# Kernel tuning notes

Measured on AMD Instinct MI355X. Metric: run time of the kernel, lower is better.

## Reference

```python
import jax, jax.numpy as jnp
import numpy as np

B, T, C, H = 4, 2048, 1024, 16
HD = C // H  # head dim = 64


def setup_inputs() -> dict:
    key = jax.random.key(0)
    k1, k2, k3 = jax.random.split(key, 3)
    scale_in = 1.0 / np.sqrt(C)
    return {
        "x": jax.random.normal(k1, (B, T, C), dtype=jnp.float32),
        "W_attn": jax.random.normal(k2, (C, 3 * C), dtype=jnp.float32) * scale_in,
        "b_attn": jnp.zeros((3 * C,), dtype=jnp.float32),
        "W_proj": jax.random.normal(k3, (C, C), dtype=jnp.float32) * scale_in,
        "b_proj": jnp.zeros((C,), dtype=jnp.float32),
    }


def reference(x, W_attn, b_attn, W_proj, b_proj):
    Bx, Tx, Cx = x.shape
    qkv = x @ W_attn + b_attn                      # [B,T,3C]
    q, k, v = jnp.split(qkv, 3, axis=-1)           # each [B,T,C]
    # [B,T,C] -> [B,H,T,HD]
    q = q.reshape(Bx, Tx, H, HD).transpose(0, 2, 1, 3)
    k = k.reshape(Bx, Tx, H, HD).transpose(0, 2, 1, 3)
    v = v.reshape(Bx, Tx, H, HD).transpose(0, 2, 1, 3)
    att = jnp.einsum("bhqd,bhkd->bhqk", q, k) * (1.0 / np.sqrt(HD))
    causal = jnp.tril(jnp.ones((Tx, Tx), dtype=bool))  # [T,T]
    att = jnp.where(causal[None, None, :, :], att, jnp.float32(-jnp.inf))
    att = jax.nn.softmax(att, axis=-1)
    y = jnp.einsum("bhqk,bhkd->bhqd", att, v)      # [B,H,T,HD]
    y = y.transpose(0, 2, 1, 3).reshape(Bx, Tx, Cx)
    return y @ W_proj + b_proj
```

## Files before the change

kernel.cpp:

```cpp
#include <hip/hip_runtime.h>

typedef _Float16 f16;
typedef __attribute__((ext_vector_type(8))) _Float16 h8;
typedef __attribute__((ext_vector_type(4))) _Float16 h4;
typedef __attribute__((ext_vector_type(4))) float f4;
typedef __attribute__((ext_vector_type(16))) float f16x;
typedef __attribute__((ext_vector_type(4))) unsigned u4;

#define MFMA(a, b, c) __builtin_amdgcn_mfma_f32_16x16x32_f16(a, b, c, 0, 0, 0)
#define MFMA32(a, b, c) __builtin_amdgcn_mfma_f32_32x32x16_f16(a, b, c, 0, 0, 0)

#define QSCALE 0.18033688011112042f

__device__ __forceinline__ void gload16(const void* g, void* l) {
    __builtin_amdgcn_global_load_lds((const __attribute__((address_space(1))) void*)g,
                                     (__attribute__((address_space(3))) void*)l, 16, 0, 0);
}

__device__ __forceinline__ float fexp2(float x) {
    float r;
    asm("v_exp_f32 %0, %1" : "=v"(r) : "v"(x));
    return r;
}

__device__ __forceinline__ unsigned pkh(float a, float b) {
    auto r = __builtin_amdgcn_cvt_pkrtz(a, b);
    return __builtin_bit_cast(unsigned, r);
}

__device__ __forceinline__ void plswap(unsigned& a, unsigned& b) {
    asm volatile("v_permlane32_swap_b32 %0, %1" : "+v"(a), "+v"(b));
}


__global__ __launch_bounds__(256) void cvt_f16_kernel(const float* __restrict__ in,
                                                      f16* __restrict__ out, int n8) {
    int i = blockIdx.x * blockDim.x + threadIdx.x;
    if (i >= n8) return;
    const float4* p = (const float4*)in + (size_t)i * 2;
    float4 a = p[0], b = p[1];
    h8 o;
    o[0] = (f16)a.x; o[1] = (f16)a.y; o[2] = (f16)a.z; o[3] = (f16)a.w;
    o[4] = (f16)b.x; o[5] = (f16)b.y; o[6] = (f16)b.z; o[7] = (f16)b.w;
    *((h8*)out + i) = o;
}

__global__ __launch_bounds__(256) void transpose_cvt(const float* __restrict__ in,
                                                     f16* __restrict__ out, int R, int Cc) {
    __shared__ float tile[32][33];
    int tx = threadIdx.x, ty = threadIdx.y;
    int c0 = blockIdx.x * 32, r0 = blockIdx.y * 32;
#pragma unroll
    for (int k = 0; k < 32; k += 8)
        tile[ty + k][tx] = in[(size_t)(r0 + ty + k) * Cc + c0 + tx];
    __syncthreads();
#pragma unroll
    for (int k = 0; k < 32; k += 8)
        out[(size_t)(c0 + ty + k) * R + r0 + tx] = (f16)tile[tx][ty + k];
}


__device__ __forceinline__ void gemm_core(const f16* __restrict__ A, const f16* __restrict__ Bt,
                                          int K, int m0, int n0,
                                          f16* lA, f16* lB, f4 acc[4][4]) {
    const int tid = threadIdx.x, lane = tid & 63, wave = tid >> 6;
    const int wm = (wave >> 1) * 64, wn = (wave & 1) * 64;
    for (int k0 = 0; k0 < K; k0 += 64) {
        __syncthreads();
#pragma unroll
        for (int i = 0; i < 4; i++) {
            int s = i * 256 + wave * 64 + lane;
            int row = s >> 3;
            int gc = ((s & 7) ^ (row & 7)) * 8;
            gload16(A + (size_t)(m0 + row) * K + k0 + gc, lA + (i * 256 + wave * 64) * 8);
        }
#pragma unroll
        for (int i = 0; i < 4; i++) {
            int s = i * 256 + wave * 64 + lane;
            int row = s >> 3;
            int gc = ((s & 7) ^ (row & 7)) * 8;
            gload16(Bt + (size_t)(n0 + row) * K + k0 + gc, lB + (i * 256 + wave * 64) * 8);
        }
        __syncthreads();
#pragma unroll
        for (int kk = 0; kk < 2; kk++) {
            h8 af[4], bg[4];
#pragma unroll
            for (int im = 0; im < 4; im++) {
                int row = wm + im * 16 + (lane & 15);
                int pc = (kk * 4 + (lane >> 4)) ^ (row & 7);
                af[im] = *(const h8*)(lA + row * 64 + pc * 8);
            }
#pragma unroll
            for (int in = 0; in < 4; in++) {
                int row = wn + in * 16 + (lane & 15);
                int pc = (kk * 4 + (lane >> 4)) ^ (row & 7);
                bg[in] = *(const h8*)(lB + row * 64 + pc * 8);
            }
#pragma unroll
            for (int im = 0; im < 4; im++)
#pragma unroll
                for (int in = 0; in < 4; in++)
                    acc[im][in] = MFMA(af[im], bg[in], acc[im][in]);
        }
    }
}


__global__ __launch_bounds__(256) void qkv_gemm(const f16* __restrict__ A, const f16* __restrict__ Bt,
                                                const float* __restrict__ bias,
                                                f16* __restrict__ Qo, f16* __restrict__ Ko,
                                                f16* __restrict__ Vo) {
    __shared__ f16 lA[128 * 64], lB[128 * 64];
    f4 acc[4][4];
    const f4 zz = {0.f, 0.f, 0.f, 0.f};
#pragma unroll
    for (int i = 0; i < 4; i++)
#pragma unroll
        for (int j = 0; j < 4; j++) acc[i][j] = zz;

    const int swz = (blockIdx.x & 7) * 192 + (blockIdx.x >> 3);
    const int nb = swz % 24, mb = swz / 24;
    gemm_core(A, Bt, 1024, mb * 128, nb * 128, lA, lB, acc);

    const int lane = threadIdx.x & 63, wave = threadIdx.x >> 6;
    const int wm = (wave >> 1) * 64, wn = (wave & 1) * 64;
#pragma unroll
    for (int im = 0; im < 4; im++) {
        int m4 = mb * 128 + wm + im * 16 + (lane >> 4) * 4;
        int b = m4 >> 11, t0 = m4 & 2047;
#pragma unroll
        for (int in = 0; in < 4; in++) {
            int n = nb * 128 + wn + in * 16 + (lane & 15);
            float bb = bias[n];
            int sec = n >> 10, cc = n & 1023, hh = cc >> 6, d = cc & 63;
            if (sec == 2) {
                h4 pv;
#pragma unroll
                for (int r = 0; r < 4; r++) pv[r] = (f16)(acc[im][in][r] + bb);
                *(h4*)(Vo + ((size_t)(b * 16 + hh) * 64 + d) * 2048 + t0) = pv;
            } else {
                f16* dst = sec ? Ko : Qo;
                float sc = sec ? 1.0f : QSCALE;
                size_t base = ((size_t)(b * 16 + hh) * 2048 + t0) * 64 + d;
#pragma unroll
                for (int r = 0; r < 4; r++)
                    dst[base + (size_t)r * 64] = (f16)((acc[im][in][r] + bb) * sc);
            }
        }
    }
}


__global__ __launch_bounds__(256) void proj_gemm(const f16* __restrict__ A, const f16* __restrict__ Bt,
                                                 const float* __restrict__ bias,
                                                 float* __restrict__ out) {
    __shared__ f16 lA[128 * 64], lB[128 * 64];
    f4 acc[4][4];
    const f4 zz = {0.f, 0.f, 0.f, 0.f};
#pragma unroll
    for (int i = 0; i < 4; i++)
#pragma unroll
        for (int j = 0; j < 4; j++) acc[i][j] = zz;

    const int swz = (blockIdx.x & 7) * 64 + (blockIdx.x >> 3);
    const int nb = swz & 7, mb = swz >> 3;
    gemm_core(A, Bt, 1024, mb * 128, nb * 128, lA, lB, acc);

    const int lane = threadIdx.x & 63, wave = threadIdx.x >> 6;
    const int wm = (wave >> 1) * 64, wn = (wave & 1) * 64;
#pragma unroll
    for (int im = 0; im < 4; im++) {
        int m4 = mb * 128 + wm + im * 16 + (lane >> 4) * 4;
#pragma unroll
        for (int in = 0; in < 4; in++) {
            int n = nb * 128 + wn + in * 16 + (lane & 15);
            float bb = bias[n];
#pragma unroll
            for (int r = 0; r < 4; r++)
                out[(size_t)(m4 + r) * 1024 + n] = acc[im][in][r] + bb;
        }
    }
}


#define ASM_VMCNT(N) asm volatile("s_waitcnt vmcnt(" #N ")" ::: "memory")

__device__ __forceinline__ void attn_tile(int k0, bool last, bool stage_next,
                                          int lane, int hi, int ln,
                                          const f16* __restrict__ Kb, const f16* __restrict__ Vb,
                                          const f16* lKcur, f16* lKnxt,
                                          const h8 (&qf)[4], h8 (&vf)[2][2], h8 (&vfn)[2][2],
                                          float& mrun, float& lpart, f16x& y0, f16x& y1) {
    if (stage_next) {
#pragma unroll
        for (int i = 0; i < 4; i++) {
            int s = i * 64 + lane;
            int row = s >> 3;
            int gc = ((s & 7) ^ (row & 7)) * 8;
            gload16(Kb + (size_t)(k0 + 32 + row) * 64 + gc, lKnxt + i * 512);
        }
#pragma unroll
        for (int ks = 0; ks < 2; ks++)
#pragma unroll
            for (int j = 0; j < 2; j++)
                vfn[ks][j] = *(const h8*)(Vb + (size_t)(j * 32 + ln) * 2048 + (k0 + 32) +
                                          ks * 16 + hi * 8);
        ASM_VMCNT(8);
    } else {
        ASM_VMCNT(0);
    }
    __builtin_amdgcn_sched_barrier(0);

    f16x s0;
#pragma unroll
    for (int r = 0; r < 16; r++) s0[r] = 0.f;
    __builtin_amdgcn_s_setprio(1);
#pragma unroll
    for (int dd = 0; dd < 4; dd++) {
        const int c = (dd * 2 + hi) ^ (ln & 7);
        h8 ka = *(const h8*)(lKcur + ln * 64 + c * 8);
        s0 = MFMA32(ka, qf[dd], s0);
    }
    __builtin_amdgcn_s_setprio(0);

    if (last) {
#pragma unroll
        for (int r = 0; r < 16; r++) {
            int kl = (r & 3) + 8 * (r >> 2) + 4 * hi;
            if (kl > ln) s0[r] = -3e38f;
        }
    }

    float vmax = s0[0];
#pragma unroll
    for (int r = 1; r < 16; r++) vmax = fmaxf(vmax, s0[r]);
    vmax = fmaxf(vmax, __shfl_xor(vmax, 32));
    if (!__all(vmax <= mrun + 8.0f)) {
        float mnew = fmaxf(mrun, vmax);
        float sc = fexp2(mrun - mnew);
        lpart *= sc;
        mrun = mnew;
#pragma unroll
        for (int r = 0; r < 16; r++) {
            float scy = __shfl(sc, (r & 3) + 8 * (r >> 2) + 4 * hi);
            y0[r] *= scy;
            y1[r] *= scy;
        }
    }
    float ls = 0.f;
#pragma unroll
    for (int r = 0; r < 16; r++) {
        float p = fexp2(s0[r] - mrun);
        s0[r] = p;
        ls += p;
    }
    lpart += ls;

    h8 pa[2];
    {
        unsigned a0 = pkh(s0[0], s0[1]), a1 = pkh(s0[2], s0[3]);
        unsigned b0 = pkh(s0[4], s0[5]), b1 = pkh(s0[6], s0[7]);
        plswap(a0, b0); plswap(a1, b1);
        u4 w0; w0[0] = a0; w0[1] = a1; w0[2] = b0; w0[3] = b1;
        pa[0] = __builtin_bit_cast(h8, w0);
        unsigned c0 = pkh(s0[8], s0[9]), c1 = pkh(s0[10], s0[11]);
        unsigned d0 = pkh(s0[12], s0[13]), d1 = pkh(s0[14], s0[15]);
        plswap(c0, d0); plswap(c1, d1);
        u4 w1; w1[0] = c0; w1[1] = c1; w1[2] = d0; w1[3] = d1;
        pa[1] = __builtin_bit_cast(h8, w1);
    }

    __builtin_amdgcn_s_setprio(1);
#pragma unroll
    for (int ks = 0; ks < 2; ks++) {
        y0 = MFMA32(pa[ks], vf[ks][0], y0);
        y1 = MFMA32(pa[ks], vf[ks][1], y1);
    }
    __builtin_amdgcn_s_setprio(0);
}

__global__ __launch_bounds__(64) void attn_kernel(const f16* __restrict__ Q,
                                                  const f16* __restrict__ K,
                                                  const f16* __restrict__ Vg,
                                                  f16* __restrict__ O) {
    __shared__ f16 lK[2][2048];
    const int lane = threadIdx.x;
    const int hi = lane >> 5, ln = lane & 31;
    const int bh = blockIdx.x & 63;
    const int p = (int)(blockIdx.x >> 6);
    const f16* Qb = Q + (size_t)bh * 2048 * 64;
    const f16* Kb = K + (size_t)bh * 2048 * 64;
    const f16* Vb = Vg + (size_t)bh * 64 * 2048;
    const int b = bh >> 4, hh = bh & 15;

    for (int ph = 0; ph < 2; ph++) {
        const int qt = ph ? p : 63 - p;
        const int qw = qt * 32;

        h8 qf[4];
#pragma unroll
        for (int dd = 0; dd < 4; dd++)
            qf[dd] = *(const h8*)(Qb + (size_t)(qw + ln) * 64 + dd * 16 + hi * 8);

        float mrun = -3e38f, lpart = 0.f;
        f16x y0, y1;
#pragma unroll
        for (int r = 0; r < 16; r++) { y0[r] = 0.f; y1[r] = 0.f; }

        const int nt = qt + 1;

        h8 vfA[2][2], vfB[2][2];
#pragma unroll
        for (int i = 0; i < 4; i++) {
            int s = i * 64 + lane;
            int row = s >> 3;
            int gc = ((s & 7) ^ (row & 7)) * 8;
            gload16(Kb + (size_t)row * 64 + gc, &lK[0][i * 512]);
        }
#pragma unroll
        for (int ks = 0; ks < 2; ks++)
#pragma unroll
            for (int j = 0; j < 2; j++)
                vfA[ks][j] = *(const h8*)(Vb + (size_t)(j * 32 + ln) * 2048 + ks * 16 + hi * 8);

        for (int it = 0; it < nt; it += 2) {
            attn_tile(it * 32, it == nt - 1, it + 1 < nt, lane, hi, ln, Kb, Vb,
                      &lK[0][0], &lK[1][0], qf, vfA, vfB, mrun, lpart, y0, y1);
            if (it + 1 < nt)
                attn_tile((it + 1) * 32, it + 1 == nt - 1, it + 2 < nt, lane, hi, ln, Kb, Vb,
                          &lK[1][0], &lK[0][0], qf, vfB, vfA, mrun, lpart, y0, y1);
        }

        float lT = lpart + __shfl_xor(lpart, 32);
        float inv = 1.0f / lT;
#pragma unroll
        for (int r = 0; r < 16; r++) {
            int crow = (r & 3) + 8 * (r >> 2) + 4 * hi;
            float invr = __shfl(inv, crow);
            size_t base = ((size_t)(b * 2048 + qw + crow)) * 1024 + hh * 64 + ln;
            O[base] = (f16)(y0[r] * invr);
            O[base + 32] = (f16)(y1[r] * invr);
        }
    }
}


extern "C" void kernel_launch(void* const* d_in, const int* in_sizes, int n_in,
                              void* d_out, int out_size, void* d_ws, size_t ws_size,
                              hipStream_t stream) {
    const float* x      = (const float*)d_in[0];
    const float* W_attn = (const float*)d_in[1];
    const float* b_attn = (const float*)d_in[2];
    const float* W_proj = (const float*)d_in[3];
    const float* b_proj = (const float*)d_in[4];
    float* out = (float*)d_out;

    char* ws = (char*)d_ws;
    f16* xb  = (f16*)ws;
    f16* Wat = (f16*)(ws + 16777216);
    f16* Wpt = (f16*)(ws + 16777216 + 6291456);
    f16* Vt  = (f16*)(ws + 16777216 + 6291456 + 2097152);
    f16* Qs  = (f16*)d_out;
    f16* Ks  = (f16*)((char*)d_out + 16777216);

    cvt_f16_kernel<<<4096, 256, 0, stream>>>(x, xb, 1048576);
    transpose_cvt<<<dim3(96, 32), dim3(32, 8), 0, stream>>>(W_attn, Wat, 1024, 3072);
    transpose_cvt<<<dim3(32, 32), dim3(32, 8), 0, stream>>>(W_proj, Wpt, 1024, 1024);
    qkv_gemm<<<1536, 256, 0, stream>>>(xb, Wat, b_attn, Qs, Ks, Vt);
    attn_kernel<<<2048, 64, 0, stream>>>(Qs, Ks, Vt, xb);
    proj_gemm<<<512, 256, 0, stream>>>(xb, Wpt, b_proj, out);
}
```

Measured before the change: 206.8 us.

## Process 64-key tiles per attention step and load V inside the tile

The causal attention loop now handles 64 keys per step instead of 32, computing two score tiles per step and masking the diagonal tile against absolute query positions. The K staging buffer doubles to 64 rows, and V fragments for the current tile are loaded at the top of each step rather than prefetched a tile ahead, with a vmcnt wait placed just before the PV MFMAs. The aim is to halve the number of online-softmax max/rescale passes and loop iterations and to issue more MFMAs per step. In exchange, V latency is hidden only by the QK and softmax work of the same step, register pressure rises, and up to 32 extra masked keys are computed on the diagonal.

```diff
diff --git a/kernel.cpp b/kernel.cpp
--- a/kernel.cpp
+++ b/kernel.cpp
@@ -186,55 +186,62 @@
 
 #define ASM_VMCNT(N) asm volatile("s_waitcnt vmcnt(" #N ")" ::: "memory")
 
-__device__ __forceinline__ void attn_tile(int k0, bool last, bool stage_next,
-                                          int lane, int hi, int ln,
-                                          const f16* __restrict__ Kb, const f16* __restrict__ Vb,
-                                          const f16* lKcur, f16* lKnxt,
-                                          const h8 (&qf)[4], h8 (&vf)[2][2], h8 (&vfn)[2][2],
-                                          float& mrun, float& lpart, f16x& y0, f16x& y1) {
+__device__ __forceinline__ void attn_tile64(int k0, bool last, bool stage_next,
+                                            int lane, int hi, int ln, int qw,
+                                            const f16* __restrict__ Kb,
+                                            const f16* __restrict__ Vb,
+                                            const f16* lKcur, f16* lKnxt,
+                                            const h8 (&qf)[4],
+                                            float& mrun, float& lpart, f16x& y0, f16x& y1) {
+    const f16* Vt = Vb + k0;
+    h8 vf[4][2];
+#pragma unroll
+    for (int ks = 0; ks < 4; ks++)
+#pragma unroll
+        for (int j = 0; j < 2; j++)
+            vf[ks][j] = *(const h8*)(Vt + (size_t)(j * 32 + ln) * 2048 + ks * 16 + hi * 8);
+
     if (stage_next) {
 #pragma unroll
-        for (int i = 0; i < 4; i++) {
+        for (int i = 0; i < 8; i++) {
             int s = i * 64 + lane;
             int row = s >> 3;
             int gc = ((s & 7) ^ (row & 7)) * 8;
-            gload16(Kb + (size_t)(k0 + 32 + row) * 64 + gc, lKnxt + i * 512);
-        }
-#pragma unroll
-        for (int ks = 0; ks < 2; ks++)
-#pragma unroll
-            for (int j = 0; j < 2; j++)
-                vfn[ks][j] = *(const h8*)(Vb + (size_t)(j * 32 + ln) * 2048 + (k0 + 32) +
-                                          ks * 16 + hi * 8);
+            gload16(Kb + (size_t)(k0 + 64 + row) * 64 + gc, lKnxt + i * 512);
+        }
+        ASM_VMCNT(16);
+    } else {
         ASM_VMCNT(8);
-    } else {
-        ASM_VMCNT(0);
     }
     __builtin_amdgcn_sched_barrier(0);
 
-    f16x s0;
-#pragma unroll
-    for (int r = 0; r < 16; r++) s0[r] = 0.f;
+    f16x s0, s1;
+#pragma unroll
+    for (int r = 0; r < 16; r++) { s0[r] = 0.f; s1[r] = 0.f; }
     __builtin_amdgcn_s_setprio(1);
 #pragma unroll
     for (int dd = 0; dd < 4; dd++) {
         const int c = (dd * 2 + hi) ^ (ln & 7);
         h8 ka = *(const h8*)(lKcur + ln * 64 + c * 8);
+        h8 kb = *(const h8*)(lKcur + (32 + ln) * 64 + c * 8);
         s0 = MFMA32(ka, qf[dd], s0);
+        s1 = MFMA32(kb, qf[dd], s1);
     }
     __builtin_amdgcn_s_setprio(0);
 
     if (last) {
+        const int qg = qw + ln;
 #pragma unroll
         for (int r = 0; r < 16; r++) {
             int kl = (r & 3) + 8 * (r >> 2) + 4 * hi;
-            if (kl > ln) s0[r] = -3e38f;
-        }
-    }
-
-    float vmax = s0[0];
-#pragma unroll
-    for (int r = 1; r < 16; r++) vmax = fmaxf(vmax, s0[r]);
+            if (k0 + kl > qg) s0[r] = -3e38f;
+            if (k0 + 32 + kl > qg) s1[r] = -3e38f;
+        }
+    }
+
+    float vmax = fmaxf(s0[0], s1[0]);
+#pragma unroll
+    for (int r = 1; r < 16; r++) vmax = fmaxf(vmax, fmaxf(s0[r], s1[r]));
     vmax = fmaxf(vmax, __shfl_xor(vmax, 32));
     if (!__all(vmax <= mrun + 8.0f)) {
         float mnew = fmaxf(mrun, vmax);
@@ -251,13 +258,14 @@
     float ls = 0.f;
 #pragma unroll
     for (int r = 0; r < 16; r++) {
-        float p = fexp2(s0[r] - mrun);
-        s0[r] = p;
-        ls += p;
+        float p0 = fexp2(s0[r] - mrun);
+        float p1 = fexp2(s1[r] - mrun);
+        s0[r] = p0; s1[r] = p1;
+        ls += p0 + p1;
     }
     lpart += ls;
 
-    h8 pa[2];
+    h8 pa[4];
     {
         unsigned a0 = pkh(s0[0], s0[1]), a1 = pkh(s0[2], s0[3]);
         unsigned b0 = pkh(s0[4], s0[5]), b1 = pkh(s0[6], s0[7]);
@@ -269,11 +277,24 @@
         plswap(c0, d0); plswap(c1, d1);
         u4 w1; w1[0] = c0; w1[1] = c1; w1[2] = d0; w1[3] = d1;
         pa[1] = __builtin_bit_cast(h8, w1);
-    }
+        unsigned e0 = pkh(s1[0], s1[1]), e1 = pkh(s1[2], s1[3]);
+        unsigned f0 = pkh(s1[4], s1[5]), f1 = pkh(s1[6], s1[7]);
+        plswap(e0, f0); plswap(e1, f1);
+        u4 w2; w2[0] = e0; w2[1] = e1; w2[2] = f0; w2[3] = f1;
+        pa[2] = __builtin_bit_cast(h8, w2);
+        unsigned g0 = pkh(s1[8], s1[9]), g1 = pkh(s1[10], s1[11]);
+        unsigned h0 = pkh(s1[12], s1[13]), h1 = pkh(s1[14], s1[15]);
+        plswap(g0, h0); plswap(g1, h1);
+        u4 w3; w3[0] = g0; w3[1] = g1; w3[2] = h0; w3[3] = h1;
+        pa[3] = __builtin_bit_cast(h8, w3);
+    }
+
+    if (stage_next) { ASM_VMCNT(8); } else { ASM_VMCNT(0); }
+    __builtin_amdgcn_sched_barrier(0);
 
     __builtin_amdgcn_s_setprio(1);
 #pragma unroll
-    for (int ks = 0; ks < 2; ks++) {
+    for (int ks = 0; ks < 4; ks++) {
         y0 = MFMA32(pa[ks], vf[ks][0], y0);
         y1 = MFMA32(pa[ks], vf[ks][1], y1);
     }
@@ -284,7 +305,7 @@
                                                   const f16* __restrict__ K,
                                                   const f16* __restrict__ Vg,
                                                   f16* __restrict__ O) {
-    __shared__ f16 lK[2][2048];
+    __shared__ f16 lK[2][4096];
     const int lane = threadIdx.x;
     const int hi = lane >> 5, ln = lane & 31;
     const int bh = blockIdx.x & 63;
@@ -308,28 +329,22 @@
 #pragma unroll
         for (int r = 0; r < 16; r++) { y0[r] = 0.f; y1[r] = 0.f; }
 
-        const int nt = qt + 1;
-
-        h8 vfA[2][2], vfB[2][2];
-#pragma unroll
-        for (int i = 0; i < 4; i++) {
+        const int nt = (qt >> 1) + 1;
+
+#pragma unroll
+        for (int i = 0; i < 8; i++) {
             int s = i * 64 + lane;
             int row = s >> 3;
             int gc = ((s & 7) ^ (row & 7)) * 8;
             gload16(Kb + (size_t)row * 64 + gc, &lK[0][i * 512]);
         }
-#pragma unroll
-        for (int ks = 0; ks < 2; ks++)
-#pragma unroll
-            for (int j = 0; j < 2; j++)
-                vfA[ks][j] = *(const h8*)(Vb + (size_t)(j * 32 + ln) * 2048 + ks * 16 + hi * 8);
 
         for (int it = 0; it < nt; it += 2) {
-            attn_tile(it * 32, it == nt - 1, it + 1 < nt, lane, hi, ln, Kb, Vb,
-                      &lK[0][0], &lK[1][0], qf, vfA, vfB, mrun, lpart, y0, y1);
+            attn_tile64(it * 64, it == nt - 1, it + 1 < nt, lane, hi, ln, qw, Kb, Vb,
+                        &lK[0][0], &lK[1][0], qf, mrun, lpart, y0, y1);
             if (it + 1 < nt)
-                attn_tile((it + 1) * 32, it + 1 == nt - 1, it + 2 < nt, lane, hi, ln, Kb, Vb,
-                          &lK[1][0], &lK[0][0], qf, vfB, vfA, mrun, lpart, y0, y1);
+                attn_tile64((it + 1) * 64, it + 1 == nt - 1, it + 2 < nt, lane, hi, ln, qw,
+                            Kb, Vb, &lK[1][0], &lK[0][0], qf, mrun, lpart, y0, y1);
         }
 
         float lT = lpart + __shfl_xor(lpart, 32);
```

Measured after the change: 241.6 us. 16.8% more time.

## Split attention KV range across two waves with flash-decoding style merge

Applied to the files above, without the earlier changes.

Each attention block now runs two waves that each process half of the key/value tiles for the same query tile, with separate LDS double buffers. Wave 0 writes its partial output, running max and sum to shared memory, and wave 1 rescales and combines both partials before writing the result. This doubles the parallelism per query tile to shorten the serial KV loop and improve latency hiding. In exchange it adds LDS traffic, two block barriers per phase, and leaves wave 0 idle during the merge.

```diff
diff --git a/kernel.cpp b/kernel.cpp
--- a/kernel.cpp
+++ b/kernel.cpp
@@ -280,12 +280,13 @@
     __builtin_amdgcn_s_setprio(0);
 }
 
-__global__ __launch_bounds__(64) void attn_kernel(const f16* __restrict__ Q,
-                                                  const f16* __restrict__ K,
-                                                  const f16* __restrict__ Vg,
-                                                  f16* __restrict__ O) {
-    __shared__ f16 lK[2][2048];
-    const int lane = threadIdx.x;
+__global__ __launch_bounds__(128) void attn_kernel(const f16* __restrict__ Q,
+                                                   const f16* __restrict__ K,
+                                                   const f16* __restrict__ Vg,
+                                                   f16* __restrict__ O) {
+    __shared__ f16 lK[2][2][2048];
+    __shared__ float xml[2][64];
+    const int tid = threadIdx.x, lane = tid & 63, wave = tid >> 6;
     const int hi = lane >> 5, ln = lane & 31;
     const int bh = blockIdx.x & 63;
     const int p = (int)(blockIdx.x >> 6);
@@ -293,10 +294,15 @@
     const f16* Kb = K + (size_t)bh * 2048 * 64;
     const f16* Vb = Vg + (size_t)bh * 64 * 2048;
     const int b = bh >> 4, hh = bh & 15;
+    f16* myK = &lK[wave][0][0];
 
     for (int ph = 0; ph < 2; ph++) {
         const int qt = ph ? p : 63 - p;
         const int qw = qt * 32;
+        const int nt = qt + 1;
+        const int h = (nt + 1) >> 1;
+        const int gs = wave ? h : 0;
+        const int ge = wave ? nt : h;
 
         h8 qf[4];
 #pragma unroll
@@ -308,40 +314,60 @@
 #pragma unroll
         for (int r = 0; r < 16; r++) { y0[r] = 0.f; y1[r] = 0.f; }
 
-        const int nt = qt + 1;
-
         h8 vfA[2][2], vfB[2][2];
-#pragma unroll
-        for (int i = 0; i < 4; i++) {
-            int s = i * 64 + lane;
-            int row = s >> 3;
-            int gc = ((s & 7) ^ (row & 7)) * 8;
-            gload16(Kb + (size_t)row * 64 + gc, &lK[0][i * 512]);
-        }
-#pragma unroll
-        for (int ks = 0; ks < 2; ks++)
-#pragma unroll
-            for (int j = 0; j < 2; j++)
-                vfA[ks][j] = *(const h8*)(Vb + (size_t)(j * 32 + ln) * 2048 + ks * 16 + hi * 8);
-
-        for (int it = 0; it < nt; it += 2) {
-            attn_tile(it * 32, it == nt - 1, it + 1 < nt, lane, hi, ln, Kb, Vb,
-                      &lK[0][0], &lK[1][0], qf, vfA, vfB, mrun, lpart, y0, y1);
-            if (it + 1 < nt)
-                attn_tile((it + 1) * 32, it + 1 == nt - 1, it + 2 < nt, lane, hi, ln, Kb, Vb,
-                          &lK[1][0], &lK[0][0], qf, vfB, vfA, mrun, lpart, y0, y1);
+        if (gs < ge) {
+#pragma unroll
+            for (int i = 0; i < 4; i++) {
+                int s = i * 64 + lane;
+                int row = s >> 3;
+                int gc = ((s & 7) ^ (row & 7)) * 8;
+                gload16(Kb + (size_t)(gs * 32 + row) * 64 + gc, myK + i * 512);
+            }
+#pragma unroll
+            for (int ks = 0; ks < 2; ks++)
+#pragma unroll
+                for (int j = 0; j < 2; j++)
+                    vfA[ks][j] = *(const h8*)(Vb + (size_t)(j * 32 + ln) * 2048 + gs * 32 +
+                                              ks * 16 + hi * 8);
+
+            for (int g = gs; g < ge; g += 2) {
+                attn_tile(g * 32, g == nt - 1, g + 1 < ge, lane, hi, ln, Kb, Vb,
+                          myK, myK + 2048, qf, vfA, vfB, mrun, lpart, y0, y1);
+                if (g + 1 < ge)
+                    attn_tile((g + 1) * 32, g + 1 == nt - 1, g + 2 < ge, lane, hi, ln, Kb, Vb,
+                              myK + 2048, myK, qf, vfB, vfA, mrun, lpart, y0, y1);
+            }
         }
 
         float lT = lpart + __shfl_xor(lpart, 32);
-        float inv = 1.0f / lT;
-#pragma unroll
-        for (int r = 0; r < 16; r++) {
-            int crow = (r & 3) + 8 * (r >> 2) + 4 * hi;
-            float invr = __shfl(inv, crow);
-            size_t base = ((size_t)(b * 2048 + qw + crow)) * 1024 + hh * 64 + ln;
-            O[base] = (f16)(y0[r] * invr);
-            O[base + 32] = (f16)(y1[r] * invr);
-        }
+        float* yb = (float*)&lK[0][0][0];
+        if (wave == 0) {
+#pragma unroll
+            for (int r = 0; r < 16; r++) {
+                yb[r * 64 + lane] = y0[r];
+                yb[1024 + r * 64 + lane] = y1[r];
+            }
+            xml[0][lane] = mrun;
+            xml[1][lane] = lT;
+        }
+        __syncthreads();
+        if (wave == 1) {
+            float m0 = xml[0][lane], l0 = xml[1][lane];
+            float m = fmaxf(m0, mrun);
+            float a0 = fexp2(m0 - m), a1 = fexp2(mrun - m);
+            float inv = 1.0f / (l0 * a0 + lT * a1);
+#pragma unroll
+            for (int r = 0; r < 16; r++) {
+                int crow = (r & 3) + 8 * (r >> 2) + 4 * hi;
+                float a0r = __shfl(a0, crow);
+                float a1r = __shfl(a1, crow);
+                float invr = __shfl(inv, crow);
+                size_t base = ((size_t)(b * 2048 + qw + crow)) * 1024 + hh * 64 + ln;
+                O[base] = (f16)((yb[r * 64 + lane] * a0r + y0[r] * a1r) * invr);
+                O[base + 32] = (f16)((yb[1024 + r * 64 + lane] * a0r + y1[r] * a1r) * invr);
+            }
+        }
+        __syncthreads();
     }
 }
 
@@ -368,6 +394,6 @@
     transpose_cvt<<<dim3(96, 32), dim3(32, 8), 0, stream>>>(W_attn, Wat, 1024, 3072);
     transpose_cvt<<<dim3(32, 32), dim3(32, 8), 0, stream>>>(W_proj, Wpt, 1024, 1024);
     qkv_gemm<<<1536, 256, 0, stream>>>(xb, Wat, b_attn, Qs, Ks, Vt);
-    attn_kernel<<<2048, 64, 0, stream>>>(Qs, Ks, Vt, xb);
+    attn_kernel<<<2048, 128, 0, stream>>>(Qs, Ks, Vt, xb);
     proj_gemm<<<512, 256, 0, stream>>>(xb, Wpt, b_proj, out);
 }
```

Measured after the change: 238.1 us. 15.1% more time.
